# Kernel optimization log

Hardware: AMD Instinct MI355X
Metric: run time of the kernel (lower is better)

## Reference

```python
import jax, jax.numpy as jnp
import numpy as np
from jax.scipy.special import logsumexp

B, T, H, S = 32, 2000, 256, 63  # batch, time steps, hidden dim, num_states (=num_classes)


def setup_inputs() -> dict:
    key = jax.random.key(0)
    ks = jax.random.split(key, 5)
    return {
        "ctc_logits": jax.random.normal(ks[0], (B, T, S), dtype=jnp.float32),
        "frame_embeddings": jax.random.normal(ks[1], (B, T, H), dtype=jnp.float32),
        "keyword_tokens": jax.random.randint(ks[2], (B, 32), 0, S),
        "W1": jax.random.normal(ks[3], (2 * H, H), dtype=jnp.float32) * 0.02,
        "b1": jnp.zeros((H,), dtype=jnp.float32),
        "W2": jax.random.normal(ks[4], (H, S), dtype=jnp.float32) * 0.02,
        "b2": jnp.zeros((S,), dtype=jnp.float32),
    }


def reference(ctc_logits, frame_embeddings, keyword_tokens, W1, b1, W2, b2):
    Bv, Tv, Sv = ctc_logits.shape
    logp = jax.nn.log_softmax(ctc_logits, axis=-1)  # (B,T,S)

    # transition scores for frame pair (t, t-1) <-> trans_all[t-1], batched over all t at once
    pairs = jnp.concatenate([frame_embeddings[:, 1:], frame_embeddings[:, :-1]], axis=-1)  # (B,T-1,2H)
    h = jax.nn.relu(jnp.einsum("bti,ij->btj", pairs, W1) + b1)
    trans = jnp.einsum("bti,ij->btj", h, W2) + b2  # (B,T-1,S)

    lp_t = jnp.swapaxes(logp, 0, 1)   # (T,B,S)
    tr_t = jnp.swapaxes(trans, 0, 1)  # (T-1,B,S)

    # forward recursion
    f0 = jnp.zeros((Bv, Sv), dtype=logp.dtype).at[:, 0].set(
        logp[jnp.arange(Bv), 0, keyword_tokens[:, 0]])

    def fstep(f_prev, x):
        lp, tr = x  # each (B,S)
        # [b,j,s] = f_prev[b,j] + lp[b,s] + tr[b,s]; reduce over j (prev state)
        scores = f_prev[:, :, None] + lp[:, None, :] + tr[:, None, :]
        f = logsumexp(scores, axis=1)
        return f, f

    _, f_rest = jax.lax.scan(fstep, f0, (lp_t[1:], tr_t))
    fwd = jnp.concatenate([f0[None], f_rest], axis=0)  # (T,B,S)

    # backward recursion (reverse scan); backward at t uses pair (t+1, t) = trans[t]
    bT = jnp.zeros((Bv, Sv), dtype=logp.dtype)

    def bstep(b_next, x):
        lp, tr = x  # lp = logp[t+1], tr = trans[t]
        # [b,s,k] = b_next[b,k] + lp[b,s] + tr[b,s]; reduce over k (next state)
        scores = b_next[:, None, :] + lp[:, :, None] + tr[:, :, None]
        b = logsumexp(scores, axis=2)
        return b, b

    _, b_rest = jax.lax.scan(bstep, bT, (lp_t[1:], tr_t), reverse=True)
    bwd = jnp.concatenate([b_rest, bT[None]], axis=0)  # (T,B,S)

    alignments = jax.nn.softmax(jnp.swapaxes(fwd + bwd, 0, 1), axis=-1)  # (B,T,S)
    return alignments
```

## Files before the change

kernel.cpp:

```cpp
#include <hip/hip_runtime.h>
#include <stdint.h>

#define NB 32
#define NT 2000
#define NH 256
#define NS 63
#define LDSROW 264

typedef __attribute__((ext_vector_type(8))) short bf16x8;
typedef __attribute__((ext_vector_type(4))) float f32x4;

__device__ inline unsigned short f2bf(float f) {
  union { float f; uint32_t u; } v; v.f = f;
  return (unsigned short)((v.u + 0x7fffu + ((v.u >> 16) & 1u)) >> 16);
}
__device__ inline unsigned int pk2(float a, float b) {
  return (unsigned int)f2bf(a) | ((unsigned int)f2bf(b) << 16);
}
__device__ inline bf16x8 pack8(const float* g) {
  union { bf16x8 v; unsigned int u[4]; } c;
  c.u[0] = pk2(g[0], g[1]); c.u[1] = pk2(g[2], g[3]);
  c.u[2] = pk2(g[4], g[5]); c.u[3] = pk2(g[6], g[7]);
  return c.v;
}

__device__ inline unsigned int pk2_hw(float a, float b) {
  unsigned int r;
  asm("v_cvt_pk_bf16_f32 %0, %1, %2" : "=v"(r) : "v"(a), "v"(b));
  return r;
}
__device__ inline unsigned short cvt1_hw(float a) {
  unsigned int r;
  asm("v_cvt_pk_bf16_f32 %0, %1, %1" : "=v"(r) : "v"(a));
  return (unsigned short)r;
}

#define NSLOT1 (16 * 4 * 4 * 64)
#define NSLOT2 (8 * 4 * 64)
#define WS_NEEDED ((size_t)(NSLOT1 + NSLOT2) * 16)

__global__ __launch_bounds__(256) void prep_weights(
    const float* __restrict__ W1, const float* __restrict__ W2,
    unsigned short* __restrict__ w1f, unsigned short* __restrict__ w2f) {
  const int tid = blockIdx.x * 256 + threadIdx.x;
  if (tid < NSLOT1) {
    const int lane = tid & 63;
    const int quad = lane >> 4, l16 = lane & 15;
    int r = tid >> 6;
    const int tn = r & 3; r >>= 2;
    const int wv = r & 3; r >>= 2;
    const int km = r;
    const int kb = (km >> 3) * 256 + (km & 7) * 32 + quad * 8;
    const int n = wv * 64 + tn * 16 + l16;
    ushort4 lo, hi;
    lo.x = f2bf(W1[(size_t)(kb + 0) * NH + n]);
    lo.y = f2bf(W1[(size_t)(kb + 1) * NH + n]);
    lo.z = f2bf(W1[(size_t)(kb + 2) * NH + n]);
    lo.w = f2bf(W1[(size_t)(kb + 3) * NH + n]);
    hi.x = f2bf(W1[(size_t)(kb + 4) * NH + n]);
    hi.y = f2bf(W1[(size_t)(kb + 5) * NH + n]);
    hi.z = f2bf(W1[(size_t)(kb + 6) * NH + n]);
    hi.w = f2bf(W1[(size_t)(kb + 7) * NH + n]);
    *(ushort4*)&w1f[(size_t)tid * 8] = lo;
    *(ushort4*)&w1f[(size_t)tid * 8 + 4] = hi;
  } else if (tid < NSLOT1 + NSLOT2) {
    const int t2 = tid - NSLOT1;
    const int lane = t2 & 63;
    const int quad = lane >> 4, l16 = lane & 15;
    const int tn = (t2 >> 6) & 3;
    const int ks = t2 >> 8;
    const int kb = ks * 32 + quad * 8;
    const int n = tn * 16 + l16;
    ushort4 lo = {0, 0, 0, 0}, hi = {0, 0, 0, 0};
    if (n < NS) {
      lo.x = f2bf(W2[(size_t)(kb + 0) * NS + n]);
      lo.y = f2bf(W2[(size_t)(kb + 1) * NS + n]);
      lo.z = f2bf(W2[(size_t)(kb + 2) * NS + n]);
      lo.w = f2bf(W2[(size_t)(kb + 3) * NS + n]);
      hi.x = f2bf(W2[(size_t)(kb + 4) * NS + n]);
      hi.y = f2bf(W2[(size_t)(kb + 5) * NS + n]);
      hi.z = f2bf(W2[(size_t)(kb + 6) * NS + n]);
      hi.w = f2bf(W2[(size_t)(kb + 7) * NS + n]);
    }
    *(ushort4*)&w2f[(size_t)t2 * 8] = lo;
    *(ushort4*)&w2f[(size_t)t2 * 8 + 4] = hi;
  }
}

template <bool PACKED>
__global__ __launch_bounds__(256, 4) void fused_kernel(
    const float* __restrict__ E, const float* __restrict__ logits,
    const int* __restrict__ kw,
    const float* __restrict__ W1, const float* __restrict__ W2,
    const unsigned short* __restrict__ w1f, const unsigned short* __restrict__ w2f,
    const float* __restrict__ b1, const float* __restrict__ b2,
    float* __restrict__ out) {
  const int b = blockIdx.y;
  const int a0 = blockIdx.x * 63;
  const int base = a0 - 1;
  const int tid = threadIdx.x;
  const int w = tid >> 6;
  const int lane = tid & 63;
  const int quad = lane >> 4;
  const int l16 = lane & 15;
  const int n0 = w * 64;

  __shared__ unsigned short lds[65 * LDSROW];
  float* TRf = (float*)lds;

  const float* Eb = E + (size_t)b * NT * NH;
  const float* lb = logits + (size_t)b * NT * NS;

  #pragma unroll
  for (int it = 0; it < 16; ++it) {
    const int row = it * 4 + w;
    int tr = base + row;
    tr = (tr < 0) ? 0 : (tr > NT - 1 ? NT - 1 : tr);
    float4 v = *(const float4*)&Eb[(size_t)tr * NH + (lane << 2)];
    uint2 o;
    o.x = pk2_hw(v.x, v.y); o.y = pk2_hw(v.z, v.w);
    *(uint2*)&lds[row * LDSROW + (lane << 2)] = o;
  }
  if (tid < 64) {
    int tr = base + 64; if (tr > NT - 1) tr = NT - 1;
    float4 v = *(const float4*)&Eb[(size_t)tr * NH + (lane << 2)];
    uint2 o;
    o.x = pk2_hw(v.x, v.y); o.y = pk2_hw(v.z, v.w);
    *(uint2*)&lds[64 * LDSROW + (lane << 2)] = o;
  }
  __syncthreads();

  f32x4 acc[4][4];
  #pragma unroll
  for (int tm = 0; tm < 4; ++tm)
    #pragma unroll
    for (int tn = 0; tn < 4; ++tn) acc[tm][tn] = (f32x4){0.f, 0.f, 0.f, 0.f};

  if constexpr (PACKED) {
    const unsigned short* wbase = w1f + (size_t)(((w << 2) * 64) + lane) * 8;
#define W1F_AT(KM, TN) \
  (*(const bf16x8*)(wbase + ((size_t)((((KM) << 4) + (TN))) << 9)))
    bf16x8 cb0 = W1F_AT(0, 0), cb1 = W1F_AT(0, 1);
    bf16x8 cb2 = W1F_AT(0, 2), cb3 = W1F_AT(0, 3);
    #pragma unroll
    for (int km = 0; km < 16; ++km) {
      bf16x8 nb0, nb1, nb2, nb3;
      if (km < 15) {
        nb0 = W1F_AT(km + 1, 0); nb1 = W1F_AT(km + 1, 1);
        nb2 = W1F_AT(km + 1, 2); nb3 = W1F_AT(km + 1, 3);
      }
      const int aoff = (km >> 3) ? 0 : 1;
      bf16x8 af[4];
      #pragma unroll
      for (int tm = 0; tm < 4; ++tm)
        af[tm] = *(const bf16x8*)&lds[(tm * 16 + l16 + aoff) * LDSROW +
                                      (km & 7) * 32 + quad * 8];
      #pragma unroll
      for (int tm = 0; tm < 4; ++tm)
        acc[tm][0] = __builtin_amdgcn_mfma_f32_16x16x32_bf16(af[tm], cb0, acc[tm][0], 0, 0, 0);
      #pragma unroll
      for (int tm = 0; tm < 4; ++tm)
        acc[tm][1] = __builtin_amdgcn_mfma_f32_16x16x32_bf16(af[tm], cb1, acc[tm][1], 0, 0, 0);
      #pragma unroll
      for (int tm = 0; tm < 4; ++tm)
        acc[tm][2] = __builtin_amdgcn_mfma_f32_16x16x32_bf16(af[tm], cb2, acc[tm][2], 0, 0, 0);
      #pragma unroll
      for (int tm = 0; tm < 4; ++tm)
        acc[tm][3] = __builtin_amdgcn_mfma_f32_16x16x32_bf16(af[tm], cb3, acc[tm][3], 0, 0, 0);
      if (km < 15) { cb0 = nb0; cb1 = nb1; cb2 = nb2; cb3 = nb3; }
    }
#undef W1F_AT
  } else {
    const float* w1p = W1 + (size_t)(quad * 8) * NH + n0 + l16;
    #pragma unroll
    for (int km = 0; km < 16; ++km) {
      const int hk = (km >> 3) * 256 + (km & 7) * 32;
      const int aoff = (km >> 3) ? 0 : 1;
      bf16x8 af[4];
      #pragma unroll
      for (int tm = 0; tm < 4; ++tm)
        af[tm] = *(const bf16x8*)&lds[(tm * 16 + l16 + aoff) * LDSROW +
                                      (km & 7) * 32 + quad * 8];
      float g[8], gn[8];
      #pragma unroll
      for (int j = 0; j < 8; ++j) g[j] = w1p[(size_t)(hk + j) * NH];
      #pragma unroll
      for (int tn = 0; tn < 4; ++tn) {
        if (tn < 3) {
          #pragma unroll
          for (int j = 0; j < 8; ++j)
            gn[j] = w1p[(size_t)(hk + j) * NH + (tn + 1) * 16];
        }
        bf16x8 bq = pack8(g);
        #pragma unroll
        for (int tm = 0; tm < 4; ++tm)
          acc[tm][tn] = __builtin_amdgcn_mfma_f32_16x16x32_bf16(
              af[tm], bq, acc[tm][tn], 0, 0, 0);
        if (tn < 3) {
          #pragma unroll
          for (int j = 0; j < 8; ++j) g[j] = gn[j];
        }
      }
    }
  }
  __syncthreads();

  #pragma unroll
  for (int tn = 0; tn < 4; ++tn) {
    float b1v = b1[n0 + tn * 16 + l16];
    #pragma unroll
    for (int tm = 0; tm < 4; ++tm)
      #pragma unroll
      for (int r = 0; r < 4; ++r) {
        float hv = fmaxf(acc[tm][tn][r] + b1v, 0.f);
        lds[(tm * 16 + quad * 4 + r) * LDSROW + n0 + tn * 16 + l16] = cvt1_hw(hv);
      }
  }
  __syncthreads();

  const int m0 = w * 16;
  float lpv[16];
  #pragma unroll
  for (int tn = 0; tn < 4; ++tn) {
    const int s = tn * 16 + l16;
    const int cc = (s < NS) ? s : NS - 1;
    #pragma unroll
    for (int r = 0; r < 4; ++r) {
      int tt = a0 + m0 + quad * 4 + r;
      if (tt > NT - 1) tt = NT - 1;
      lpv[tn * 4 + r] = lb[(size_t)tt * NS + cc];
    }
  }

  f32x4 acc2[4];
  #pragma unroll
  for (int tn = 0; tn < 4; ++tn) acc2[tn] = (f32x4){0.f, 0.f, 0.f, 0.f};

  if constexpr (PACKED) {
    const unsigned short* w2base = w2f + (size_t)lane * 8;
    #pragma unroll
    for (int ks = 0; ks < 8; ++ks) {
      bf16x8 af = *(const bf16x8*)&lds[(m0 + l16) * LDSROW + ks * 32 + quad * 8];
      #pragma unroll
      for (int tn = 0; tn < 4; ++tn) {
        bf16x8 bq = *(const bf16x8*)(w2base + ((size_t)((ks << 2) + tn) << 9));
        acc2[tn] = __builtin_amdgcn_mfma_f32_16x16x32_bf16(af, bq, acc2[tn], 0, 0, 0);
      }
    }
  } else {
    #pragma unroll
    for (int ks = 0; ks < 8; ++ks) {
      const int k0 = ks * 32;
      bf16x8 af = *(const bf16x8*)&lds[(m0 + l16) * LDSROW + k0 + quad * 8];
      #pragma unroll
      for (int tn = 0; tn < 4; ++tn) {
        const int n = tn * 16 + l16;
        float g[8];
        #pragma unroll
        for (int j = 0; j < 8; ++j)
          g[j] = (n < NS) ? W2[(size_t)(k0 + quad * 8 + j) * NS + n] : 0.f;
        bf16x8 bq = pack8(g);
        acc2[tn] = __builtin_amdgcn_mfma_f32_16x16x32_bf16(af, bq, acc2[tn], 0, 0, 0);
      }
    }
  }
  __syncthreads();

  #pragma unroll
  for (int tn = 0; tn < 4; ++tn) {
    const int s = tn * 16 + l16;
    const float b2v = (s < NS) ? b2[s] : 0.f;
    #pragma unroll
    for (int r = 0; r < 4; ++r)
      TRf[(m0 + quad * 4 + r) * 68 + s] = acc2[tn][r] + b2v + lpv[tn * 4 + r];
  }
  __syncthreads();

  for (int rr = 0; rr < 16; ++rr) {
    const int j = m0 + rr;
    const int t = a0 + j;
    if (j == 63 || t > NT - 1) continue;
    float sc;
    if (t == 0) {
      float v = (lane < NS) ? lb[lane] : -1e30f;
      float m = v;
      #pragma unroll
      for (int o = 32; o > 0; o >>= 1) m = fmaxf(m, __shfl_xor(m, o));
      float ee = (lane < NS) ? __expf(v - m) : 0.f;
      float ss = ee;
      #pragma unroll
      for (int o = 32; o > 0; o >>= 1) ss += __shfl_xor(ss, o);
      const float lse = m + __logf(ss);
      const float f00 = lb[kw[b * 32]] - lse;
      sc = ((lane == 0) ? f00 : 0.f) + TRf[68 + lane];
    } else if (t == NT - 1) {
      sc = TRf[j * 68 + lane];
    } else {
      sc = TRf[j * 68 + lane] + TRf[(j + 1) * 68 + lane];
    }
    float e = (lane < NS) ? __expf(sc) : 0.f;
    float s = e;
    #pragma unroll
    for (int o = 32; o > 0; o >>= 1) s += __shfl_xor(s, o);
    const float sinv = __builtin_amdgcn_rcpf(s);
    if (lane < NS) out[((size_t)b * NT + t) * NS + lane] = e * sinv;
  }
}

extern "C" void kernel_launch(void* const* d_in, const int* in_sizes, int n_in,
                              void* d_out, int out_size, void* d_ws, size_t ws_size,
                              hipStream_t stream) {
  const float* logits = (const float*)d_in[0];
  const float* E      = (const float*)d_in[1];
  const int*   kw     = (const int*)d_in[2];
  const float* W1     = (const float*)d_in[3];
  const float* b1     = (const float*)d_in[4];
  const float* W2     = (const float*)d_in[5];
  const float* b2     = (const float*)d_in[6];
  float* out = (float*)d_out;

  dim3 g(32, NB);

  if (ws_size >= WS_NEEDED && d_ws != nullptr) {
    unsigned short* w1f = (unsigned short*)d_ws;
    unsigned short* w2f = w1f + (size_t)NSLOT1 * 8;
    prep_weights<<<dim3((NSLOT1 + NSLOT2) / 256), 256, 0, stream>>>(W1, W2, w1f, w2f);
    fused_kernel<true><<<g, 256, 0, stream>>>(E, logits, kw, W1, W2, w1f, w2f,
                                              b1, b2, out);
  } else {
    fused_kernel<false><<<g, 256, 0, stream>>>(E, logits, kw, W1, W2, nullptr,
                                               nullptr, b1, b2, out);
  }
}
```

Baseline: 137.2 us.

## Halve per-block time tile to 31 frames and batch softmax reductions

Each block now covers 31 output frames instead of 63, so the grid grows from 32 to 65 blocks per batch row. LDS use drops to 33 rows and the accumulator tiles shrink, which allows launch_bounds to ask for 5 blocks per CU. The second GEMM runs only on the first two waves. The final softmax now computes 8 rows per wave with interleaved shuffle reductions, and the t==0 row is handled separately. The halo row and the W1 reads are now spread over twice as many blocks, adding redundant loads and making the second GEMM imbalanced across waves.

```diff
diff --git a/kernel.cpp b/kernel.cpp
--- a/kernel.cpp
+++ b/kernel.cpp
@@ -6,6 +6,9 @@
 #define NH 256
 #define NS 63
 #define LDSROW 264
+#define EROWS 33
+#define TOUT 31
+#define NTB 65
 
 typedef __attribute__((ext_vector_type(8))) short bf16x8;
 typedef __attribute__((ext_vector_type(4))) float f32x4;
@@ -88,7 +91,7 @@
 }
 
 template <bool PACKED>
-__global__ __launch_bounds__(256, 4) void fused_kernel(
+__global__ __launch_bounds__(256, 5) void fused_kernel(
     const float* __restrict__ E, const float* __restrict__ logits,
     const int* __restrict__ kw,
     const float* __restrict__ W1, const float* __restrict__ W2,
@@ -96,7 +99,7 @@
     const float* __restrict__ b1, const float* __restrict__ b2,
     float* __restrict__ out) {
   const int b = blockIdx.y;
-  const int a0 = blockIdx.x * 63;
+  const int a0 = blockIdx.x * TOUT;
   const int base = a0 - 1;
   const int tid = threadIdx.x;
   const int w = tid >> 6;
@@ -105,14 +108,14 @@
   const int l16 = lane & 15;
   const int n0 = w * 64;
 
-  __shared__ unsigned short lds[65 * LDSROW];
+  __shared__ unsigned short lds[EROWS * LDSROW];
   float* TRf = (float*)lds;
 
   const float* Eb = E + (size_t)b * NT * NH;
   const float* lb = logits + (size_t)b * NT * NS;
 
   #pragma unroll
-  for (int it = 0; it < 16; ++it) {
+  for (int it = 0; it < 8; ++it) {
     const int row = it * 4 + w;
     int tr = base + row;
     tr = (tr < 0) ? 0 : (tr > NT - 1 ? NT - 1 : tr);
@@ -122,17 +125,18 @@
     *(uint2*)&lds[row * LDSROW + (lane << 2)] = o;
   }
   if (tid < 64) {
-    int tr = base + 64; if (tr > NT - 1) tr = NT - 1;
+    int tr = base + 32;
+    tr = (tr < 0) ? 0 : (tr > NT - 1 ? NT - 1 : tr);
     float4 v = *(const float4*)&Eb[(size_t)tr * NH + (lane << 2)];
     uint2 o;
     o.x = pk2_hw(v.x, v.y); o.y = pk2_hw(v.z, v.w);
-    *(uint2*)&lds[64 * LDSROW + (lane << 2)] = o;
-  }
-  __syncthreads();
-
-  f32x4 acc[4][4];
-  #pragma unroll
-  for (int tm = 0; tm < 4; ++tm)
+    *(uint2*)&lds[32 * LDSROW + (lane << 2)] = o;
+  }
+  __syncthreads();
+
+  f32x4 acc[2][4];
+  #pragma unroll
+  for (int tm = 0; tm < 2; ++tm)
     #pragma unroll
     for (int tn = 0; tn < 4; ++tn) acc[tm][tn] = (f32x4){0.f, 0.f, 0.f, 0.f};
 
@@ -150,22 +154,22 @@
         nb2 = W1F_AT(km + 1, 2); nb3 = W1F_AT(km + 1, 3);
       }
       const int aoff = (km >> 3) ? 0 : 1;
-      bf16x8 af[4];
-      #pragma unroll
-      for (int tm = 0; tm < 4; ++tm)
+      bf16x8 af[2];
+      #pragma unroll
+      for (int tm = 0; tm < 2; ++tm)
         af[tm] = *(const bf16x8*)&lds[(tm * 16 + l16 + aoff) * LDSROW +
                                       (km & 7) * 32 + quad * 8];
       #pragma unroll
-      for (int tm = 0; tm < 4; ++tm)
+      for (int tm = 0; tm < 2; ++tm)
         acc[tm][0] = __builtin_amdgcn_mfma_f32_16x16x32_bf16(af[tm], cb0, acc[tm][0], 0, 0, 0);
       #pragma unroll
-      for (int tm = 0; tm < 4; ++tm)
+      for (int tm = 0; tm < 2; ++tm)
         acc[tm][1] = __builtin_amdgcn_mfma_f32_16x16x32_bf16(af[tm], cb1, acc[tm][1], 0, 0, 0);
       #pragma unroll
-      for (int tm = 0; tm < 4; ++tm)
+      for (int tm = 0; tm < 2; ++tm)
         acc[tm][2] = __builtin_amdgcn_mfma_f32_16x16x32_bf16(af[tm], cb2, acc[tm][2], 0, 0, 0);
       #pragma unroll
-      for (int tm = 0; tm < 4; ++tm)
+      for (int tm = 0; tm < 2; ++tm)
         acc[tm][3] = __builtin_amdgcn_mfma_f32_16x16x32_bf16(af[tm], cb3, acc[tm][3], 0, 0, 0);
       if (km < 15) { cb0 = nb0; cb1 = nb1; cb2 = nb2; cb3 = nb3; }
     }
@@ -176,9 +180,9 @@
     for (int km = 0; km < 16; ++km) {
       const int hk = (km >> 3) * 256 + (km & 7) * 32;
       const int aoff = (km >> 3) ? 0 : 1;
-      bf16x8 af[4];
-      #pragma unroll
-      for (int tm = 0; tm < 4; ++tm)
+      bf16x8 af[2];
+      #pragma unroll
+      for (int tm = 0; tm < 2; ++tm)
         af[tm] = *(const bf16x8*)&lds[(tm * 16 + l16 + aoff) * LDSROW +
                                       (km & 7) * 32 + quad * 8];
       float g[8], gn[8];
@@ -193,7 +197,7 @@
         }
         bf16x8 bq = pack8(g);
         #pragma unroll
-        for (int tm = 0; tm < 4; ++tm)
+        for (int tm = 0; tm < 2; ++tm)
           acc[tm][tn] = __builtin_amdgcn_mfma_f32_16x16x32_bf16(
               af[tm], bq, acc[tm][tn], 0, 0, 0);
         if (tn < 3) {
@@ -209,7 +213,7 @@
   for (int tn = 0; tn < 4; ++tn) {
     float b1v = b1[n0 + tn * 16 + l16];
     #pragma unroll
-    for (int tm = 0; tm < 4; ++tm)
+    for (int tm = 0; tm < 2; ++tm)
       #pragma unroll
       for (int r = 0; r < 4; ++r) {
         float hv = fmaxf(acc[tm][tn][r] + b1v, 0.f);
@@ -220,90 +224,108 @@
 
   const int m0 = w * 16;
   float lpv[16];
-  #pragma unroll
-  for (int tn = 0; tn < 4; ++tn) {
-    const int s = tn * 16 + l16;
-    const int cc = (s < NS) ? s : NS - 1;
-    #pragma unroll
-    for (int r = 0; r < 4; ++r) {
-      int tt = a0 + m0 + quad * 4 + r;
-      if (tt > NT - 1) tt = NT - 1;
-      lpv[tn * 4 + r] = lb[(size_t)tt * NS + cc];
-    }
-  }
-
   f32x4 acc2[4];
-  #pragma unroll
-  for (int tn = 0; tn < 4; ++tn) acc2[tn] = (f32x4){0.f, 0.f, 0.f, 0.f};
-
-  if constexpr (PACKED) {
-    const unsigned short* w2base = w2f + (size_t)lane * 8;
-    #pragma unroll
-    for (int ks = 0; ks < 8; ++ks) {
-      bf16x8 af = *(const bf16x8*)&lds[(m0 + l16) * LDSROW + ks * 32 + quad * 8];
-      #pragma unroll
-      for (int tn = 0; tn < 4; ++tn) {
-        bf16x8 bq = *(const bf16x8*)(w2base + ((size_t)((ks << 2) + tn) << 9));
-        acc2[tn] = __builtin_amdgcn_mfma_f32_16x16x32_bf16(af, bq, acc2[tn], 0, 0, 0);
-      }
-    }
-  } else {
-    #pragma unroll
-    for (int ks = 0; ks < 8; ++ks) {
-      const int k0 = ks * 32;
-      bf16x8 af = *(const bf16x8*)&lds[(m0 + l16) * LDSROW + k0 + quad * 8];
-      #pragma unroll
-      for (int tn = 0; tn < 4; ++tn) {
-        const int n = tn * 16 + l16;
-        float g[8];
+  if (w < 2) {
+    #pragma unroll
+    for (int tn = 0; tn < 4; ++tn) {
+      const int s = tn * 16 + l16;
+      const int cc = (s < NS) ? s : NS - 1;
+      #pragma unroll
+      for (int r = 0; r < 4; ++r) {
+        int tt = a0 + m0 + quad * 4 + r;
+        if (tt > NT - 1) tt = NT - 1;
+        lpv[tn * 4 + r] = lb[(size_t)tt * NS + cc];
+      }
+    }
+    #pragma unroll
+    for (int tn = 0; tn < 4; ++tn) acc2[tn] = (f32x4){0.f, 0.f, 0.f, 0.f};
+
+    if constexpr (PACKED) {
+      const unsigned short* w2base = w2f + (size_t)lane * 8;
+      #pragma unroll
+      for (int ks = 0; ks < 8; ++ks) {
+        bf16x8 af = *(const bf16x8*)&lds[(m0 + l16) * LDSROW + ks * 32 + quad * 8];
         #pragma unroll
-        for (int j = 0; j < 8; ++j)
-          g[j] = (n < NS) ? W2[(size_t)(k0 + quad * 8 + j) * NS + n] : 0.f;
-        bf16x8 bq = pack8(g);
-        acc2[tn] = __builtin_amdgcn_mfma_f32_16x16x32_bf16(af, bq, acc2[tn], 0, 0, 0);
-      }
-    }
-  }
-  __syncthreads();
-
-  #pragma unroll
-  for (int tn = 0; tn < 4; ++tn) {
-    const int s = tn * 16 + l16;
-    const float b2v = (s < NS) ? b2[s] : 0.f;
-    #pragma unroll
-    for (int r = 0; r < 4; ++r)
-      TRf[(m0 + quad * 4 + r) * 68 + s] = acc2[tn][r] + b2v + lpv[tn * 4 + r];
-  }
-  __syncthreads();
-
-  for (int rr = 0; rr < 16; ++rr) {
-    const int j = m0 + rr;
-    const int t = a0 + j;
-    if (j == 63 || t > NT - 1) continue;
-    float sc;
-    if (t == 0) {
-      float v = (lane < NS) ? lb[lane] : -1e30f;
-      float m = v;
-      #pragma unroll
-      for (int o = 32; o > 0; o >>= 1) m = fmaxf(m, __shfl_xor(m, o));
-      float ee = (lane < NS) ? __expf(v - m) : 0.f;
-      float ss = ee;
-      #pragma unroll
-      for (int o = 32; o > 0; o >>= 1) ss += __shfl_xor(ss, o);
-      const float lse = m + __logf(ss);
-      const float f00 = lb[kw[b * 32]] - lse;
-      sc = ((lane == 0) ? f00 : 0.f) + TRf[68 + lane];
-    } else if (t == NT - 1) {
-      sc = TRf[j * 68 + lane];
+        for (int tn = 0; tn < 4; ++tn) {
+          bf16x8 bq = *(const bf16x8*)(w2base + ((size_t)((ks << 2) + tn) << 9));
+          acc2[tn] = __builtin_amdgcn_mfma_f32_16x16x32_bf16(af, bq, acc2[tn], 0, 0, 0);
+        }
+      }
     } else {
-      sc = TRf[j * 68 + lane] + TRf[(j + 1) * 68 + lane];
-    }
+      #pragma unroll
+      for (int ks = 0; ks < 8; ++ks) {
+        const int k0 = ks * 32;
+        bf16x8 af = *(const bf16x8*)&lds[(m0 + l16) * LDSROW + k0 + quad * 8];
+        #pragma unroll
+        for (int tn = 0; tn < 4; ++tn) {
+          const int n = tn * 16 + l16;
+          float g[8];
+          #pragma unroll
+          for (int j = 0; j < 8; ++j)
+            g[j] = (n < NS) ? W2[(size_t)(k0 + quad * 8 + j) * NS + n] : 0.f;
+          bf16x8 bq = pack8(g);
+          acc2[tn] = __builtin_amdgcn_mfma_f32_16x16x32_bf16(af, bq, acc2[tn], 0, 0, 0);
+        }
+      }
+    }
+  }
+  __syncthreads();
+
+  if (w < 2) {
+    #pragma unroll
+    for (int tn = 0; tn < 4; ++tn) {
+      const int s = tn * 16 + l16;
+      const float b2v = (s < NS) ? b2[s] : 0.f;
+      #pragma unroll
+      for (int r = 0; r < 4; ++r)
+        TRf[(m0 + quad * 4 + r) * 68 + s] = acc2[tn][r] + b2v + lpv[tn * 4 + r];
+    }
+  }
+  __syncthreads();
+
+  if (a0 == 0 && w == 0) {
+    float v = (lane < NS) ? lb[lane] : -1e30f;
+    float m = v;
+    #pragma unroll
+    for (int o = 32; o > 0; o >>= 1) m = fmaxf(m, __shfl_xor(m, o));
+    float ee = (lane < NS) ? __expf(v - m) : 0.f;
+    float ss = ee;
+    #pragma unroll
+    for (int o = 32; o > 0; o >>= 1) ss += __shfl_xor(ss, o);
+    const float lse = m + __logf(ss);
+    const float f00 = lb[kw[b * 32]] - lse;
+    float sc = ((lane == 0) ? f00 : 0.f) + TRf[68 + lane];
     float e = (lane < NS) ? __expf(sc) : 0.f;
     float s = e;
     #pragma unroll
     for (int o = 32; o > 0; o >>= 1) s += __shfl_xor(s, o);
-    const float sinv = __builtin_amdgcn_rcpf(s);
-    if (lane < NS) out[((size_t)b * NT + t) * NS + lane] = e * sinv;
+    if (lane < NS) out[lane + (size_t)b * NT * NS] = e * __builtin_amdgcn_rcpf(s);
+  }
+
+  const int jbase = w * 8;
+  float ev[8], sm[8];
+  #pragma unroll
+  for (int rr = 0; rr < 8; ++rr) {
+    const int j = jbase + rr;
+    const int t = a0 + j;
+    const bool valid = (j < TOUT) && (t < NT) && (t != 0);
+    float u0 = valid ? TRf[j * 68 + lane] : 0.f;
+    float u1 = (valid && t != NT - 1) ? TRf[(j + 1) * 68 + lane] : 0.f;
+    ev[rr] = (valid && lane < NS) ? __expf(u0 + u1) : 0.f;
+    sm[rr] = ev[rr];
+  }
+  #pragma unroll
+  for (int o = 32; o > 0; o >>= 1) {
+    #pragma unroll
+    for (int rr = 0; rr < 8; ++rr) sm[rr] += __shfl_xor(sm[rr], o);
+  }
+  #pragma unroll
+  for (int rr = 0; rr < 8; ++rr) {
+    const int j = jbase + rr;
+    const int t = a0 + j;
+    const bool valid = (j < TOUT) && (t < NT) && (t != 0);
+    if (valid && lane < NS)
+      out[((size_t)b * NT + t) * NS + lane] = ev[rr] * __builtin_amdgcn_rcpf(sm[rr]);
   }
 }
 
@@ -319,7 +341,7 @@
   const float* b2     = (const float*)d_in[6];
   float* out = (float*)d_out;
 
-  dim3 g(32, NB);
+  dim3 g(NTB, NB);
 
   if (ws_size >= WS_NEEDED && d_ws != nullptr) {
     unsigned short* w1f = (unsigned short*)d_ws;
```

New measurement: 144.8 us. +5.5%, slower.

## Double the per-block time tile to 127 frames using 512-thread blocks

Applied to the files above, without the earlier changes.

Each block now covers 128 staged frames and 127 output frames with eight waves instead of four. The eight waves form two row halves times four column groups, so each W1 fragment loaded from global memory feeds twice as many rows. This also reduces the share of halo frames recomputed at block edges. Shared memory moves to a dynamic allocation sized for 129 rows. The costs are half as many blocks, which leaves fewer blocks to fill the CUs, and a launch bound of 512 threads with 4 blocks that may squeeze the register budget enough to cause spills.

```diff
diff --git a/kernel.cpp b/kernel.cpp
--- a/kernel.cpp
+++ b/kernel.cpp
@@ -6,6 +6,10 @@
 #define NH 256
 #define NS 63
 #define LDSROW 264
+#define MROWS 128
+#define EROWS 129
+#define TOUT 127
+#define NTB 16
 
 typedef __attribute__((ext_vector_type(8))) short bf16x8;
 typedef __attribute__((ext_vector_type(4))) float f32x4;
@@ -88,7 +92,7 @@
 }
 
 template <bool PACKED>
-__global__ __launch_bounds__(256, 4) void fused_kernel(
+__global__ __launch_bounds__(512, 4) void fused_kernel(
     const float* __restrict__ E, const float* __restrict__ logits,
     const int* __restrict__ kw,
     const float* __restrict__ W1, const float* __restrict__ W2,
@@ -96,16 +100,19 @@
     const float* __restrict__ b1, const float* __restrict__ b2,
     float* __restrict__ out) {
   const int b = blockIdx.y;
-  const int a0 = blockIdx.x * 63;
+  const int a0 = blockIdx.x * TOUT;
   const int base = a0 - 1;
   const int tid = threadIdx.x;
   const int w = tid >> 6;
   const int lane = tid & 63;
   const int quad = lane >> 4;
   const int l16 = lane & 15;
-  const int n0 = w * 64;
-
-  __shared__ unsigned short lds[65 * LDSROW];
+  const int c = w & 3;
+  const int rh = w >> 2;
+  const int n0 = c * 64;
+  const int r0 = rh * 64;
+
+  extern __shared__ unsigned short lds[];
   float* TRf = (float*)lds;
 
   const float* Eb = E + (size_t)b * NT * NH;
@@ -113,7 +120,7 @@
 
   #pragma unroll
   for (int it = 0; it < 16; ++it) {
-    const int row = it * 4 + w;
+    const int row = it * 8 + w;
     int tr = base + row;
     tr = (tr < 0) ? 0 : (tr > NT - 1 ? NT - 1 : tr);
     float4 v = *(const float4*)&Eb[(size_t)tr * NH + (lane << 2)];
@@ -122,11 +129,11 @@
     *(uint2*)&lds[row * LDSROW + (lane << 2)] = o;
   }
   if (tid < 64) {
-    int tr = base + 64; if (tr > NT - 1) tr = NT - 1;
+    int tr = base + 128; if (tr > NT - 1) tr = NT - 1;
     float4 v = *(const float4*)&Eb[(size_t)tr * NH + (lane << 2)];
     uint2 o;
     o.x = pk2_hw(v.x, v.y); o.y = pk2_hw(v.z, v.w);
-    *(uint2*)&lds[64 * LDSROW + (lane << 2)] = o;
+    *(uint2*)&lds[128 * LDSROW + (lane << 2)] = o;
   }
   __syncthreads();
 
@@ -137,7 +144,7 @@
     for (int tn = 0; tn < 4; ++tn) acc[tm][tn] = (f32x4){0.f, 0.f, 0.f, 0.f};
 
   if constexpr (PACKED) {
-    const unsigned short* wbase = w1f + (size_t)(((w << 2) * 64) + lane) * 8;
+    const unsigned short* wbase = w1f + (size_t)(((c << 2) * 64) + lane) * 8;
 #define W1F_AT(KM, TN) \
   (*(const bf16x8*)(wbase + ((size_t)((((KM) << 4) + (TN))) << 9)))
     bf16x8 cb0 = W1F_AT(0, 0), cb1 = W1F_AT(0, 1);
@@ -153,7 +160,7 @@
       bf16x8 af[4];
       #pragma unroll
       for (int tm = 0; tm < 4; ++tm)
-        af[tm] = *(const bf16x8*)&lds[(tm * 16 + l16 + aoff) * LDSROW +
+        af[tm] = *(const bf16x8*)&lds[(r0 + tm * 16 + l16 + aoff) * LDSROW +
                                       (km & 7) * 32 + quad * 8];
       #pragma unroll
       for (int tm = 0; tm < 4; ++tm)
@@ -179,7 +186,7 @@
       bf16x8 af[4];
       #pragma unroll
       for (int tm = 0; tm < 4; ++tm)
-        af[tm] = *(const bf16x8*)&lds[(tm * 16 + l16 + aoff) * LDSROW +
+        af[tm] = *(const bf16x8*)&lds[(r0 + tm * 16 + l16 + aoff) * LDSROW +
                                       (km & 7) * 32 + quad * 8];
       float g[8], gn[8];
       #pragma unroll
@@ -213,7 +220,7 @@
       #pragma unroll
       for (int r = 0; r < 4; ++r) {
         float hv = fmaxf(acc[tm][tn][r] + b1v, 0.f);
-        lds[(tm * 16 + quad * 4 + r) * LDSROW + n0 + tn * 16 + l16] = cvt1_hw(hv);
+        lds[(r0 + tm * 16 + quad * 4 + r) * LDSROW + n0 + tn * 16 + l16] = cvt1_hw(hv);
       }
   }
   __syncthreads();
@@ -279,7 +286,7 @@
   for (int rr = 0; rr < 16; ++rr) {
     const int j = m0 + rr;
     const int t = a0 + j;
-    if (j == 63 || t > NT - 1) continue;
+    if (j == TOUT || t > NT - 1) continue;
     float sc;
     if (t == 0) {
       float v = (lane < NS) ? lb[lane] : -1e30f;
@@ -319,16 +326,17 @@
   const float* b2     = (const float*)d_in[6];
   float* out = (float*)d_out;
 
-  dim3 g(32, NB);
+  dim3 g(NTB, NB);
+  const size_t shmem = (size_t)EROWS * LDSROW * sizeof(unsigned short);
 
   if (ws_size >= WS_NEEDED && d_ws != nullptr) {
     unsigned short* w1f = (unsigned short*)d_ws;
     unsigned short* w2f = w1f + (size_t)NSLOT1 * 8;
     prep_weights<<<dim3((NSLOT1 + NSLOT2) / 256), 256, 0, stream>>>(W1, W2, w1f, w2f);
-    fused_kernel<true><<<g, 256, 0, stream>>>(E, logits, kw, W1, W2, w1f, w2f,
-                                              b1, b2, out);
+    fused_kernel<true><<<g, 512, shmem, stream>>>(E, logits, kw, W1, W2, w1f, w2f,
+                                                  b1, b2, out);
   } else {
-    fused_kernel<false><<<g, 256, 0, stream>>>(E, logits, kw, W1, W2, nullptr,
-                                               nullptr, b1, b2, out);
-  }
-}
+    fused_kernel<false><<<g, 512, shmem, stream>>>(E, logits, kw, W1, W2, nullptr,
+                                                   nullptr, b1, b2, out);
+  }
+}
```

Result: slower. 142.2 us (+3.6%).

## Use 1024-thread blocks looping over four time tiles with double-buffered embedding prefetch

Applied to the files above, without the earlier changes.

The kernel now launches 1024-thread blocks on an 8x32 grid. Each block loops over four consecutive 63-frame tiles. Embedding rows for the next tile are loaded into registers during the current tile's compute and written into a second LDS buffer, so global-load latency overlaps with MFMA work. The first GEMM is split so each of 16 waves computes a 16x64 slab. The second GEMM runs on only 4 of the 16 waves, and every wave re-fetches its W1 fragments for each tile. The trade-offs are more LDS per block (dynamic shared memory), fewer resident blocks, and idle waves during the second GEMM.

```diff
diff --git a/kernel.cpp b/kernel.cpp
--- a/kernel.cpp
+++ b/kernel.cpp
@@ -6,6 +6,9 @@
 #define NH 256
 #define NS 63
 #define LDSROW 264
+#define TILE_USH (65 * LDSROW)
+#define NTILES 4
+#define TBX 8
 
 typedef __attribute__((ext_vector_type(8))) short bf16x8;
 typedef __attribute__((ext_vector_type(4))) float f32x4;
@@ -23,7 +26,6 @@
   c.u[2] = pk2(g[4], g[5]); c.u[3] = pk2(g[6], g[7]);
   return c.v;
 }
-
 __device__ inline unsigned int pk2_hw(float a, float b) {
   unsigned int r;
   asm("v_cvt_pk_bf16_f32 %0, %1, %2" : "=v"(r) : "v"(a), "v"(b));
@@ -87,8 +89,38 @@
   }
 }
 
+
+__device__ __forceinline__ void issueE(const float* __restrict__ Eb, int base,
+                                       int w, int lane, int tid,
+                                       float4 eb[4], float4& eb4) {
+  #pragma unroll
+  for (int it = 0; it < 4; ++it) {
+    int tr = base + it * 16 + w;
+    tr = (tr < 0) ? 0 : (tr > NT - 1 ? NT - 1 : tr);
+    eb[it] = *(const float4*)&Eb[(size_t)tr * NH + (lane << 2)];
+  }
+  if (tid < 64) {
+    int tr = base + 64; if (tr > NT - 1) tr = NT - 1;
+    eb4 = *(const float4*)&Eb[(size_t)tr * NH + (lane << 2)];
+  }
+}
+__device__ __forceinline__ void writeE(unsigned short* R, int w, int lane,
+                                       int tid, const float4 eb[4],
+                                       const float4& eb4) {
+  #pragma unroll
+  for (int it = 0; it < 4; ++it) {
+    const int row = it * 16 + w;
+    uint2 o; o.x = pk2_hw(eb[it].x, eb[it].y); o.y = pk2_hw(eb[it].z, eb[it].w);
+    *(uint2*)&R[row * LDSROW + (lane << 2)] = o;
+  }
+  if (tid < 64) {
+    uint2 o; o.x = pk2_hw(eb4.x, eb4.y); o.y = pk2_hw(eb4.z, eb4.w);
+    *(uint2*)&R[64 * LDSROW + (lane << 2)] = o;
+  }
+}
+
 template <bool PACKED>
-__global__ __launch_bounds__(256, 4) void fused_kernel(
+__global__ __launch_bounds__(1024, 4) void fused_kernel(
     const float* __restrict__ E, const float* __restrict__ logits,
     const int* __restrict__ kw,
     const float* __restrict__ W1, const float* __restrict__ W2,
@@ -96,214 +128,209 @@
     const float* __restrict__ b1, const float* __restrict__ b2,
     float* __restrict__ out) {
   const int b = blockIdx.y;
-  const int a0 = blockIdx.x * 63;
-  const int base = a0 - 1;
+  const int bx = blockIdx.x;
   const int tid = threadIdx.x;
   const int w = tid >> 6;
   const int lane = tid & 63;
   const int quad = lane >> 4;
   const int l16 = lane & 15;
-  const int n0 = w * 64;
-
-  __shared__ unsigned short lds[65 * LDSROW];
-  float* TRf = (float*)lds;
+  const int c = w & 3;
+  const int rq = w >> 2;
+  const int n0 = c * 64;
+
+  extern __shared__ unsigned short lds[];
+  unsigned short* rgn0 = lds;
+  unsigned short* rgn1 = lds + TILE_USH;
+  float* U = (float*)(lds + 2 * TILE_USH);
 
   const float* Eb = E + (size_t)b * NT * NH;
   const float* lb = logits + (size_t)b * NT * NS;
 
-  #pragma unroll
-  for (int it = 0; it < 16; ++it) {
-    const int row = it * 4 + w;
-    int tr = base + row;
-    tr = (tr < 0) ? 0 : (tr > NT - 1 ? NT - 1 : tr);
-    float4 v = *(const float4*)&Eb[(size_t)tr * NH + (lane << 2)];
-    uint2 o;
-    o.x = pk2_hw(v.x, v.y); o.y = pk2_hw(v.z, v.w);
-    *(uint2*)&lds[row * LDSROW + (lane << 2)] = o;
-  }
-  if (tid < 64) {
-    int tr = base + 64; if (tr > NT - 1) tr = NT - 1;
-    float4 v = *(const float4*)&Eb[(size_t)tr * NH + (lane << 2)];
-    uint2 o;
-    o.x = pk2_hw(v.x, v.y); o.y = pk2_hw(v.z, v.w);
-    *(uint2*)&lds[64 * LDSROW + (lane << 2)] = o;
-  }
+  {
+    const int base = bx * (NTILES * 63) - 1;
+    #pragma unroll
+    for (int it = 0; it < 4; ++it) {
+      const int row = it * 16 + w;
+      int tr = base + row;
+      tr = (tr < 0) ? 0 : (tr > NT - 1 ? NT - 1 : tr);
+      float4 v = *(const float4*)&Eb[(size_t)tr * NH + (lane << 2)];
+      uint2 o; o.x = pk2_hw(v.x, v.y); o.y = pk2_hw(v.z, v.w);
+      *(uint2*)&rgn0[row * LDSROW + (lane << 2)] = o;
+    }
+    if (tid < 64) {
+      int tr = base + 64; if (tr > NT - 1) tr = NT - 1;
+      float4 v = *(const float4*)&Eb[(size_t)tr * NH + (lane << 2)];
+      uint2 o; o.x = pk2_hw(v.x, v.y); o.y = pk2_hw(v.z, v.w);
+      *(uint2*)&rgn0[64 * LDSROW + (lane << 2)] = o;
+    }
+  }
+  float4 eb[4]; float4 eb4;
+  issueE(Eb, (bx * NTILES + 1) * 63 - 1, w, lane, tid, eb, eb4);
   __syncthreads();
 
-  f32x4 acc[4][4];
-  #pragma unroll
-  for (int tm = 0; tm < 4; ++tm)
+  for (int k = 0; k < NTILES; ++k) {
+    const int a0 = (bx * NTILES + k) * 63;
+    unsigned short* Rc = (k & 1) ? rgn1 : rgn0;
+    unsigned short* Rn = (k & 1) ? rgn0 : rgn1;
+
+    f32x4 acc[4];
     #pragma unroll
-    for (int tn = 0; tn < 4; ++tn) acc[tm][tn] = (f32x4){0.f, 0.f, 0.f, 0.f};
-
-  if constexpr (PACKED) {
-    const unsigned short* wbase = w1f + (size_t)(((w << 2) * 64) + lane) * 8;
+    for (int tn = 0; tn < 4; ++tn) acc[tn] = (f32x4){0.f, 0.f, 0.f, 0.f};
+
+    if constexpr (PACKED) {
+      const unsigned short* wbase = w1f + (size_t)(((c << 2) * 64) + lane) * 8;
 #define W1F_AT(KM, TN) \
   (*(const bf16x8*)(wbase + ((size_t)((((KM) << 4) + (TN))) << 9)))
-    bf16x8 cb0 = W1F_AT(0, 0), cb1 = W1F_AT(0, 1);
-    bf16x8 cb2 = W1F_AT(0, 2), cb3 = W1F_AT(0, 3);
+      bf16x8 cb0 = W1F_AT(0, 0), cb1 = W1F_AT(0, 1);
+      bf16x8 cb2 = W1F_AT(0, 2), cb3 = W1F_AT(0, 3);
+      #pragma unroll
+      for (int km = 0; km < 16; ++km) {
+        bf16x8 nb0, nb1, nb2, nb3;
+        if (km < 15) {
+          nb0 = W1F_AT(km + 1, 0); nb1 = W1F_AT(km + 1, 1);
+          nb2 = W1F_AT(km + 1, 2); nb3 = W1F_AT(km + 1, 3);
+        }
+        const int aoff = (km >> 3) ? 0 : 1;
+        bf16x8 af = *(const bf16x8*)&Rc[(rq * 16 + l16 + aoff) * LDSROW +
+                                        (km & 7) * 32 + quad * 8];
+        acc[0] = __builtin_amdgcn_mfma_f32_16x16x32_bf16(af, cb0, acc[0], 0, 0, 0);
+        acc[1] = __builtin_amdgcn_mfma_f32_16x16x32_bf16(af, cb1, acc[1], 0, 0, 0);
+        acc[2] = __builtin_amdgcn_mfma_f32_16x16x32_bf16(af, cb2, acc[2], 0, 0, 0);
+        acc[3] = __builtin_amdgcn_mfma_f32_16x16x32_bf16(af, cb3, acc[3], 0, 0, 0);
+        if (km < 15) { cb0 = nb0; cb1 = nb1; cb2 = nb2; cb3 = nb3; }
+      }
+#undef W1F_AT
+    } else {
+      const float* w1p = W1 + (size_t)(quad * 8) * NH + n0 + l16;
+      #pragma unroll
+      for (int km = 0; km < 16; ++km) {
+        const int hk = (km >> 3) * 256 + (km & 7) * 32;
+        const int aoff = (km >> 3) ? 0 : 1;
+        bf16x8 af = *(const bf16x8*)&Rc[(rq * 16 + l16 + aoff) * LDSROW +
+                                        (km & 7) * 32 + quad * 8];
+        float g[8], gn[8];
+        #pragma unroll
+        for (int j = 0; j < 8; ++j) g[j] = w1p[(size_t)(hk + j) * NH];
+        #pragma unroll
+        for (int tn = 0; tn < 4; ++tn) {
+          if (tn < 3) {
+            #pragma unroll
+            for (int j = 0; j < 8; ++j)
+              gn[j] = w1p[(size_t)(hk + j) * NH + (tn + 1) * 16];
+          }
+          bf16x8 bq = pack8(g);
+          acc[tn] = __builtin_amdgcn_mfma_f32_16x16x32_bf16(af, bq, acc[tn], 0, 0, 0);
+          if (tn < 3) {
+            #pragma unroll
+            for (int j = 0; j < 8; ++j) g[j] = gn[j];
+          }
+        }
+      }
+    }
+    __syncthreads();
+
+    if (k < NTILES - 1) writeE(Rn, w, lane, tid, eb, eb4);
     #pragma unroll
-    for (int km = 0; km < 16; ++km) {
-      bf16x8 nb0, nb1, nb2, nb3;
-      if (km < 15) {
-        nb0 = W1F_AT(km + 1, 0); nb1 = W1F_AT(km + 1, 1);
-        nb2 = W1F_AT(km + 1, 2); nb3 = W1F_AT(km + 1, 3);
-      }
-      const int aoff = (km >> 3) ? 0 : 1;
-      bf16x8 af[4];
-      #pragma unroll
-      for (int tm = 0; tm < 4; ++tm)
-        af[tm] = *(const bf16x8*)&lds[(tm * 16 + l16 + aoff) * LDSROW +
-                                      (km & 7) * 32 + quad * 8];
-      #pragma unroll
-      for (int tm = 0; tm < 4; ++tm)
-        acc[tm][0] = __builtin_amdgcn_mfma_f32_16x16x32_bf16(af[tm], cb0, acc[tm][0], 0, 0, 0);
-      #pragma unroll
-      for (int tm = 0; tm < 4; ++tm)
-        acc[tm][1] = __builtin_amdgcn_mfma_f32_16x16x32_bf16(af[tm], cb1, acc[tm][1], 0, 0, 0);
-      #pragma unroll
-      for (int tm = 0; tm < 4; ++tm)
-        acc[tm][2] = __builtin_amdgcn_mfma_f32_16x16x32_bf16(af[tm], cb2, acc[tm][2], 0, 0, 0);
-      #pragma unroll
-      for (int tm = 0; tm < 4; ++tm)
-        acc[tm][3] = __builtin_amdgcn_mfma_f32_16x16x32_bf16(af[tm], cb3, acc[tm][3], 0, 0, 0);
-      if (km < 15) { cb0 = nb0; cb1 = nb1; cb2 = nb2; cb3 = nb3; }
-    }
-#undef W1F_AT
-  } else {
-    const float* w1p = W1 + (size_t)(quad * 8) * NH + n0 + l16;
+    for (int tn = 0; tn < 4; ++tn) {
+      float b1v = b1[n0 + tn * 16 + l16];
+      #pragma unroll
+      for (int r = 0; r < 4; ++r) {
+        float hv = fmaxf(acc[tn][r] + b1v, 0.f);
+        Rc[(rq * 16 + quad * 4 + r) * LDSROW + n0 + tn * 16 + l16] = cvt1_hw(hv);
+      }
+    }
+    __syncthreads();
+
+    if (w < 4) {
+      const int m0 = w * 16;
+      float lpv[16];
+      #pragma unroll
+      for (int tn = 0; tn < 4; ++tn) {
+        const int s = tn * 16 + l16;
+        const int cc = (s < NS) ? s : NS - 1;
+        #pragma unroll
+        for (int r = 0; r < 4; ++r) {
+          int tt = a0 + m0 + quad * 4 + r;
+          if (tt > NT - 1) tt = NT - 1;
+          lpv[tn * 4 + r] = lb[(size_t)tt * NS + cc];
+        }
+      }
+      f32x4 acc2[4];
+      #pragma unroll
+      for (int tn = 0; tn < 4; ++tn) acc2[tn] = (f32x4){0.f, 0.f, 0.f, 0.f};
+
+      if constexpr (PACKED) {
+        const unsigned short* w2base = w2f + (size_t)lane * 8;
+        #pragma unroll
+        for (int ks = 0; ks < 8; ++ks) {
+          bf16x8 af = *(const bf16x8*)&Rc[(m0 + l16) * LDSROW + ks * 32 + quad * 8];
+          #pragma unroll
+          for (int tn = 0; tn < 4; ++tn) {
+            bf16x8 bq = *(const bf16x8*)(w2base + ((size_t)((ks << 2) + tn) << 9));
+            acc2[tn] = __builtin_amdgcn_mfma_f32_16x16x32_bf16(af, bq, acc2[tn], 0, 0, 0);
+          }
+        }
+      } else {
+        #pragma unroll
+        for (int ks = 0; ks < 8; ++ks) {
+          const int k0 = ks * 32;
+          bf16x8 af = *(const bf16x8*)&Rc[(m0 + l16) * LDSROW + k0 + quad * 8];
+          #pragma unroll
+          for (int tn = 0; tn < 4; ++tn) {
+            const int n = tn * 16 + l16;
+            float g[8];
+            #pragma unroll
+            for (int j = 0; j < 8; ++j)
+              g[j] = (n < NS) ? W2[(size_t)(k0 + quad * 8 + j) * NS + n] : 0.f;
+            bf16x8 bq = pack8(g);
+            acc2[tn] = __builtin_amdgcn_mfma_f32_16x16x32_bf16(af, bq, acc2[tn], 0, 0, 0);
+          }
+        }
+      }
+      #pragma unroll
+      for (int tn = 0; tn < 4; ++tn) {
+        const int s = tn * 16 + l16;
+        const float b2v = (s < NS) ? b2[s] : 0.f;
+        #pragma unroll
+        for (int r = 0; r < 4; ++r)
+          U[(m0 + quad * 4 + r) * 68 + s] = acc2[tn][r] + b2v + lpv[tn * 4 + r];
+      }
+    }
+    __syncthreads();
+
+    if (k < NTILES - 2)
+      issueE(Eb, (bx * NTILES + k + 2) * 63 - 1, w, lane, tid, eb, eb4);
+
     #pragma unroll
-    for (int km = 0; km < 16; ++km) {
-      const int hk = (km >> 3) * 256 + (km & 7) * 32;
-      const int aoff = (km >> 3) ? 0 : 1;
-      bf16x8 af[4];
-      #pragma unroll
-      for (int tm = 0; tm < 4; ++tm)
-        af[tm] = *(const bf16x8*)&lds[(tm * 16 + l16 + aoff) * LDSROW +
-                                      (km & 7) * 32 + quad * 8];
-      float g[8], gn[8];
-      #pragma unroll
-      for (int j = 0; j < 8; ++j) g[j] = w1p[(size_t)(hk + j) * NH];
-      #pragma unroll
-      for (int tn = 0; tn < 4; ++tn) {
-        if (tn < 3) {
-          #pragma unroll
-          for (int j = 0; j < 8; ++j)
-            gn[j] = w1p[(size_t)(hk + j) * NH + (tn + 1) * 16];
-        }
-        bf16x8 bq = pack8(g);
-        #pragma unroll
-        for (int tm = 0; tm < 4; ++tm)
-          acc[tm][tn] = __builtin_amdgcn_mfma_f32_16x16x32_bf16(
-              af[tm], bq, acc[tm][tn], 0, 0, 0);
-        if (tn < 3) {
-          #pragma unroll
-          for (int j = 0; j < 8; ++j) g[j] = gn[j];
-        }
-      }
-    }
-  }
-  __syncthreads();
-
-  #pragma unroll
-  for (int tn = 0; tn < 4; ++tn) {
-    float b1v = b1[n0 + tn * 16 + l16];
-    #pragma unroll
-    for (int tm = 0; tm < 4; ++tm)
-      #pragma unroll
-      for (int r = 0; r < 4; ++r) {
-        float hv = fmaxf(acc[tm][tn][r] + b1v, 0.f);
-        lds[(tm * 16 + quad * 4 + r) * LDSROW + n0 + tn * 16 + l16] = cvt1_hw(hv);
-      }
-  }
-  __syncthreads();
-
-  const int m0 = w * 16;
-  float lpv[16];
-  #pragma unroll
-  for (int tn = 0; tn < 4; ++tn) {
-    const int s = tn * 16 + l16;
-    const int cc = (s < NS) ? s : NS - 1;
-    #pragma unroll
-    for (int r = 0; r < 4; ++r) {
-      int tt = a0 + m0 + quad * 4 + r;
-      if (tt > NT - 1) tt = NT - 1;
-      lpv[tn * 4 + r] = lb[(size_t)tt * NS + cc];
-    }
-  }
-
-  f32x4 acc2[4];
-  #pragma unroll
-  for (int tn = 0; tn < 4; ++tn) acc2[tn] = (f32x4){0.f, 0.f, 0.f, 0.f};
-
-  if constexpr (PACKED) {
-    const unsigned short* w2base = w2f + (size_t)lane * 8;
-    #pragma unroll
-    for (int ks = 0; ks < 8; ++ks) {
-      bf16x8 af = *(const bf16x8*)&lds[(m0 + l16) * LDSROW + ks * 32 + quad * 8];
-      #pragma unroll
-      for (int tn = 0; tn < 4; ++tn) {
-        bf16x8 bq = *(const bf16x8*)(w2base + ((size_t)((ks << 2) + tn) << 9));
-        acc2[tn] = __builtin_amdgcn_mfma_f32_16x16x32_bf16(af, bq, acc2[tn], 0, 0, 0);
-      }
-    }
-  } else {
-    #pragma unroll
-    for (int ks = 0; ks < 8; ++ks) {
-      const int k0 = ks * 32;
-      bf16x8 af = *(const bf16x8*)&lds[(m0 + l16) * LDSROW + k0 + quad * 8];
-      #pragma unroll
-      for (int tn = 0; tn < 4; ++tn) {
-        const int n = tn * 16 + l16;
-        float g[8];
-        #pragma unroll
-        for (int j = 0; j < 8; ++j)
-          g[j] = (n < NS) ? W2[(size_t)(k0 + quad * 8 + j) * NS + n] : 0.f;
-        bf16x8 bq = pack8(g);
-        acc2[tn] = __builtin_amdgcn_mfma_f32_16x16x32_bf16(af, bq, acc2[tn], 0, 0, 0);
-      }
-    }
-  }
-  __syncthreads();
-
-  #pragma unroll
-  for (int tn = 0; tn < 4; ++tn) {
-    const int s = tn * 16 + l16;
-    const float b2v = (s < NS) ? b2[s] : 0.f;
-    #pragma unroll
-    for (int r = 0; r < 4; ++r)
-      TRf[(m0 + quad * 4 + r) * 68 + s] = acc2[tn][r] + b2v + lpv[tn * 4 + r];
-  }
-  __syncthreads();
-
-  for (int rr = 0; rr < 16; ++rr) {
-    const int j = m0 + rr;
-    const int t = a0 + j;
-    if (j == 63 || t > NT - 1) continue;
-    float sc;
-    if (t == 0) {
-      float v = (lane < NS) ? lb[lane] : -1e30f;
-      float m = v;
-      #pragma unroll
-      for (int o = 32; o > 0; o >>= 1) m = fmaxf(m, __shfl_xor(m, o));
-      float ee = (lane < NS) ? __expf(v - m) : 0.f;
-      float ss = ee;
-      #pragma unroll
-      for (int o = 32; o > 0; o >>= 1) ss += __shfl_xor(ss, o);
-      const float lse = m + __logf(ss);
-      const float f00 = lb[kw[b * 32]] - lse;
-      sc = ((lane == 0) ? f00 : 0.f) + TRf[68 + lane];
-    } else if (t == NT - 1) {
-      sc = TRf[j * 68 + lane];
-    } else {
-      sc = TRf[j * 68 + lane] + TRf[(j + 1) * 68 + lane];
-    }
-    float e = (lane < NS) ? __expf(sc) : 0.f;
-    float s = e;
-    #pragma unroll
-    for (int o = 32; o > 0; o >>= 1) s += __shfl_xor(s, o);
-    const float sinv = __builtin_amdgcn_rcpf(s);
-    if (lane < NS) out[((size_t)b * NT + t) * NS + lane] = e * sinv;
+    for (int rr = 0; rr < 4; ++rr) {
+      const int j = w * 4 + rr;
+      const int t = a0 + j;
+      if (j == 63 || t > NT - 1) continue;
+      float sc;
+      if (t == 0) {
+        float v = (lane < NS) ? lb[lane] : -1e30f;
+        float m = v;
+        #pragma unroll
+        for (int o = 32; o > 0; o >>= 1) m = fmaxf(m, __shfl_xor(m, o));
+        float ee = (lane < NS) ? __expf(v - m) : 0.f;
+        float ss = ee;
+        #pragma unroll
+        for (int o = 32; o > 0; o >>= 1) ss += __shfl_xor(ss, o);
+        const float lse = m + __logf(ss);
+        const float f00 = lb[kw[b * 32]] - lse;
+        sc = ((lane == 0) ? f00 : 0.f) + U[68 + lane];
+      } else if (t == NT - 1) {
+        sc = U[j * 68 + lane];
+      } else {
+        sc = U[j * 68 + lane] + U[(j + 1) * 68 + lane];
+      }
+      float e = (lane < NS) ? __expf(sc) : 0.f;
+      float s = e;
+      #pragma unroll
+      for (int o = 32; o > 0; o >>= 1) s += __shfl_xor(s, o);
+      const float sinv = __builtin_amdgcn_rcpf(s);
+      if (lane < NS) out[((size_t)b * NT + t) * NS + lane] = e * sinv;
+    }
   }
 }
 
@@ -319,16 +346,18 @@
   const float* b2     = (const float*)d_in[6];
   float* out = (float*)d_out;
 
-  dim3 g(32, NB);
+  dim3 g(TBX, NB);
+  const size_t shmem = (size_t)2 * TILE_USH * sizeof(unsigned short)
+                     + (size_t)64 * 68 * sizeof(float);
 
   if (ws_size >= WS_NEEDED && d_ws != nullptr) {
     unsigned short* w1f = (unsigned short*)d_ws;
     unsigned short* w2f = w1f + (size_t)NSLOT1 * 8;
     prep_weights<<<dim3((NSLOT1 + NSLOT2) / 256), 256, 0, stream>>>(W1, W2, w1f, w2f);
-    fused_kernel<true><<<g, 256, 0, stream>>>(E, logits, kw, W1, W2, w1f, w2f,
-                                              b1, b2, out);
+    fused_kernel<true><<<g, 1024, shmem, stream>>>(E, logits, kw, W1, W2, w1f, w2f,
+                                                   b1, b2, out);
   } else {
-    fused_kernel<false><<<g, 256, 0, stream>>>(E, logits, kw, W1, W2, nullptr,
-                                               nullptr, b1, b2, out);
-  }
-}
+    fused_kernel<false><<<g, 1024, shmem, stream>>>(E, logits, kw, W1, W2, nullptr,
+                                                    nullptr, b1, b2, out);
+  }
+}
```

Result: slower. 435.9 us (+217.7%).
